# Kernel optimization log

Measured on AMD Instinct MI355X. Metric: run time of the kernel, lower is better.

The kernel has to match this reference:

```python
import jax, jax.numpy as jnp
import numpy as np

B, N, L, S, H, E = 4, 8, 512, 512, 8, 64  # e == d (value head dim)


def setup_inputs() -> dict:
    key = jax.random.key(0)
    ks = jax.random.split(key, 6)
    shp_q = (B, N, L, H, E)
    shp_kv = (B, N, S, H, E)
    return {
        "q_re": jax.random.normal(ks[0], shp_q, dtype=jnp.float32),
        "q_im": jax.random.normal(ks[1], shp_q, dtype=jnp.float32),
        "k_re": jax.random.normal(ks[2], shp_kv, dtype=jnp.float32),
        "k_im": jax.random.normal(ks[3], shp_kv, dtype=jnp.float32),
        "v_re": jax.random.normal(ks[4], shp_kv, dtype=jnp.float32),
        "v_im": jax.random.normal(ks[5], shp_kv, dtype=jnp.float32),
    }


def reference(q_re, q_im, k_re, k_im, v_re, v_im):
    # complex_mul('bnlhe,bnshe->bnhls', q, k):
    #   real = qr.kr - qi.ki ; imag = qr.ki - qi.kr  (note: NOT standard +; faithful to source)
    s_re = (jnp.einsum('bnlhe,bnshe->bnhls', q_re, k_re)
            - jnp.einsum('bnlhe,bnshe->bnhls', q_im, k_im))
    s_im = (jnp.einsum('bnlhe,bnshe->bnhls', q_re, k_im)
            - jnp.einsum('bnlhe,bnshe->bnhls', q_im, k_re))
    # softmax over |scores| along key axis s (no 1/sqrt(e) scaling in source)
    mag = jnp.sqrt(s_re * s_re + s_im * s_im)
    attn = jax.nn.softmax(mag, axis=-1)  # [b,n,h,l,s]; dropout = identity (eval)
    # scores are real-valued after softmax; complex_mul with zero imag reduces to:
    v_out_re = jnp.einsum('bnhls,bnshd->bnlhd', attn, v_re)
    v_out_im = jnp.einsum('bnhls,bnshd->bnlhd', attn, v_im)
    # stack real/imag (torch returns complex tensor) -> [2,b,n,l,h,d]
    return jnp.stack((v_out_re, v_out_im), axis=0)
```

## Files before the change

### kernel.cpp

```cpp
#include <hip/hip_runtime.h>
#include <hip/hip_fp16.h>

typedef _Float16 half8 __attribute__((ext_vector_type(8)));
typedef _Float16 half4 __attribute__((ext_vector_type(4)));
typedef __fp16  fp16x2 __attribute__((ext_vector_type(2)));
typedef float f32x4 __attribute__((ext_vector_type(4)));

#define BB 4
#define NB 8
#define LL 512
#define SS 512
#define HH 8
#define EE 64
#define ROWSTRIDE (HH * EE)

__device__ __forceinline__ unsigned pkh(float a, float b) {
    union { fp16x2 h; unsigned u; } c;
    c.h = __builtin_amdgcn_cvt_pkrtz(a, b);
    return c.u;
}


__global__ __launch_bounds__(512, 4) void cattn_kernel(
    const float* __restrict__ qre, const float* __restrict__ qim,
    const float* __restrict__ kre, const float* __restrict__ kim,
    const float* __restrict__ vre, const float* __restrict__ vim,
    float* __restrict__ out)
{
    __shared__ __align__(16) _Float16 KtRe[2][64 * 64];
    __shared__ __align__(16) _Float16 KtIm[2][64 * 64];
    __shared__ __align__(16) _Float16 VtRe[2][64 * 64];
    __shared__ __align__(16) _Float16 VtIm[2][64 * 64];
    __shared__ __align__(16) _Float16 Pbuf[8][16 * 64];

    const int tid  = threadIdx.x;
    const int wave = tid >> 6;
    const int lane = tid & 63;
    const int lgrp = lane >> 4;
    const int l16  = lane & 15;

    const int bid  = blockIdx.x;
    const int nid  = (bid & 7) * 128 + (bid >> 3);
    const int lt   = nid & 3;
    const int head = nid >> 2;
    const int h    = head & 7;
    const int bn   = head >> 3;

    const size_t headQ = (size_t)bn * LL * ROWSTRIDE + (size_t)h * EE;
    const size_t headK = (size_t)bn * SS * ROWSTRIDE + (size_t)h * EE;

    float4 ka[2], kb[2];
    float4 vv[4];

    const int kEc0  = tid & 7;
    const int kS0   = (tid >> 3) & 63;
    const int vArr  = tid >> 8;
    const int vD0   = (tid & 15) * 4;
    const int vS0   = ((tid >> 4) & 15) * 4;

    auto stage_load = [&](int st) {
        const int tb = st * 64;
        {
            const float* p = kre + headK + (size_t)(tb + kS0) * ROWSTRIDE + kEc0 * 8;
            ka[0] = *(const float4*)p;
            kb[0] = *(const float4*)(p + 4);
        }
        {
            const float* p = kim + headK + (size_t)(tb + kS0) * ROWSTRIDE + kEc0 * 8;
            ka[1] = *(const float4*)p;
            kb[1] = *(const float4*)(p + 4);
        }
        {
            const float* src = vArr ? vim : vre;
            #pragma unroll
            for (int i = 0; i < 4; ++i)
                vv[i] = *(const float4*)(src + headK + (size_t)(tb + vS0 + i) * ROWSTRIDE + vD0);
        }
    };

    auto stage_write = [&](int buf) {
        #pragma unroll
        for (int it = 0; it < 2; ++it) {
            union { half8 h; unsigned u[4]; } kv;
            kv.u[0] = pkh(ka[it].x, ka[it].y);
            kv.u[1] = pkh(ka[it].z, ka[it].w);
            kv.u[2] = pkh(kb[it].x, kb[it].y);
            kv.u[3] = pkh(kb[it].z, kb[it].w);
            _Float16* base = it ? KtIm[buf] : KtRe[buf];
            *reinterpret_cast<half8*>(reinterpret_cast<char*>(base) +
                kS0 * 128 + ((kEc0 * 16) ^ ((kS0 & 7) << 4))) = kv.h;
        }
        {
            _Float16* base = vArr ? VtIm[buf] : VtRe[buf];
            #pragma unroll
            for (int dd = 0; dd < 4; ++dd) {
                int d = vD0 + dd;
                union { half4 h; unsigned u[2]; } hv;
                hv.u[0] = pkh((&vv[0].x)[dd], (&vv[1].x)[dd]);
                hv.u[1] = pkh((&vv[2].x)[dd], (&vv[3].x)[dd]);
                *reinterpret_cast<half4*>(reinterpret_cast<char*>(base) +
                    d * 128 + ((vS0 * 2) ^ ((d & 7) << 4))) = hv.h;
            }
        }
    };

    const int l0 = lt * 128 + wave * 16;
    half8 qr[2], qin[2];
    {
        size_t base = headQ + (size_t)(l0 + l16) * ROWSTRIDE + lgrp * 8;
        #pragma unroll
        for (int ec = 0; ec < 2; ++ec) {
            float4 a0 = *(const float4*)(qre + base + ec * 32);
            float4 a1 = *(const float4*)(qre + base + ec * 32 + 4);
            float4 b0 = *(const float4*)(qim + base + ec * 32);
            float4 b1 = *(const float4*)(qim + base + ec * 32 + 4);
            #pragma unroll
            for (int j = 0; j < 4; ++j) {
                qr[ec][j]      = (_Float16)((&a0.x)[j]);
                qr[ec][4 + j]  = (_Float16)((&a1.x)[j]);
                qin[ec][j]     = (_Float16)(-(&b0.x)[j]);
                qin[ec][4 + j] = (_Float16)(-(&b1.x)[j]);
            }
        }
    }

    f32x4 ore[4], oim[4];
    #pragma unroll
    for (int n = 0; n < 4; ++n) { ore[n] = (f32x4){0.f,0.f,0.f,0.f}; oim[n] = (f32x4){0.f,0.f,0.f,0.f}; }
    float m = -1e30f, lsum = 0.f;

    stage_load(0);
    stage_write(0);
    __syncthreads();

    char* Pw = reinterpret_cast<char*>(&Pbuf[wave][0]);
    const int prow = l16 * 128;
    const int pswz = (l16 & 7) << 4;

    for (int st = 0; st < 8; ++st) {
        const int cur = st & 1;
        if (st < 7) stage_load(st + 1);

        const char* KR = (const char*)KtRe[cur];
        const char* KI = (const char*)KtIm[cur];
        const char* VR = (const char*)VtRe[cur];
        const char* VI = (const char*)VtIm[cur];

        float p_[4][4];
        float tmax = 0.f;
        #pragma unroll
        for (int n = 0; n < 4; ++n) {
            int srow = n * 16 + l16;
            int rb   = srow * 128;
            int swz  = (srow & 7) << 4;
            half8 kr0 = *(const half8*)(KR + rb + ((lgrp * 16)      ^ swz));
            half8 kr1 = *(const half8*)(KR + rb + ((64 + lgrp * 16) ^ swz));
            half8 ki0 = *(const half8*)(KI + rb + ((lgrp * 16)      ^ swz));
            half8 ki1 = *(const half8*)(KI + rb + ((64 + lgrp * 16) ^ swz));
            f32x4 z = (f32x4){0.f,0.f,0.f,0.f};
            z = __builtin_amdgcn_mfma_f32_16x16x32_f16(kr0, qr[0],  z, 0, 0, 0);
            z = __builtin_amdgcn_mfma_f32_16x16x32_f16(kr1, qr[1],  z, 0, 0, 0);
            z = __builtin_amdgcn_mfma_f32_16x16x32_f16(ki0, qin[0], z, 0, 0, 0);
            z = __builtin_amdgcn_mfma_f32_16x16x32_f16(ki1, qin[1], z, 0, 0, 0);
            f32x4 w = (f32x4){0.f,0.f,0.f,0.f};
            w = __builtin_amdgcn_mfma_f32_16x16x32_f16(ki0, qr[0],  w, 0, 0, 0);
            w = __builtin_amdgcn_mfma_f32_16x16x32_f16(ki1, qr[1],  w, 0, 0, 0);
            w = __builtin_amdgcn_mfma_f32_16x16x32_f16(kr0, qin[0], w, 0, 0, 0);
            w = __builtin_amdgcn_mfma_f32_16x16x32_f16(kr1, qin[1], w, 0, 0, 0);
            #pragma unroll
            for (int r = 0; r < 4; ++r) {
                float mg = __builtin_amdgcn_sqrtf(z[r] * z[r] + w[r] * w[r]);
                p_[n][r] = mg;
                tmax = fmaxf(tmax, mg);
            }
        }

        tmax = fmaxf(tmax, __shfl_xor(tmax, 16));
        tmax = fmaxf(tmax, __shfl_xor(tmax, 32));
        float mn = fmaxf(m, tmax);
        if (__any(tmax > m)) {
            float sc = __expf(m - mn);
            lsum *= sc;
            float scr[4];
            #pragma unroll
            for (int r = 0; r < 4; ++r) scr[r] = __shfl(sc, lgrp * 4 + r);
            #pragma unroll
            for (int n = 0; n < 4; ++n)
                #pragma unroll
                for (int r = 0; r < 4; ++r) { ore[n][r] *= scr[r]; oim[n][r] *= scr[r]; }
        }
        m = mn;
        float ps = 0.f;
        #pragma unroll
        for (int n = 0; n < 4; ++n)
            #pragma unroll
            for (int r = 0; r < 4; ++r) {
                float pe = __expf(p_[n][r] - mn);
                p_[n][r] = pe;
                ps += pe;
            }
        ps += __shfl_xor(ps, 16);
        ps += __shfl_xor(ps, 32);
        lsum += ps;

        #pragma unroll
        for (int n = 0; n < 4; ++n) {
            uint2 val;
            val.x = pkh(p_[n][0], p_[n][1]);
            val.y = pkh(p_[n][2], p_[n][3]);
            *reinterpret_cast<uint2*>(Pw + prow + ((n * 32 + lgrp * 8) ^ pswz)) = val;
        }

        #pragma unroll
        for (int kc = 0; kc < 2; ++kc) {
            half8 pa = *reinterpret_cast<const half8*>(Pw + prow + ((kc * 64 + lgrp * 16) ^ pswz));
            int sb2 = (kc * 32 + lgrp * 8) * 2;
            #pragma unroll
            for (int nd = 0; nd < 4; ++nd) {
                int d  = nd * 16 + l16;
                int vo = d * 128 + (sb2 ^ ((d & 7) << 4));
                half8 vr = *(const half8*)(VR + vo);
                half8 vi = *(const half8*)(VI + vo);
                ore[nd] = __builtin_amdgcn_mfma_f32_16x16x32_f16(pa, vr, ore[nd], 0, 0, 0);
                oim[nd] = __builtin_amdgcn_mfma_f32_16x16x32_f16(pa, vi, oim[nd], 0, 0, 0);
            }
        }

        if (st < 7) stage_write(cur ^ 1);
        __syncthreads();
    }

    const size_t outImOff = (size_t)BB * NB * LL * HH * EE;
    #pragma unroll
    for (int r = 0; r < 4; ++r) {
        int lrow = l0 + lgrp * 4 + r;
        float ls  = __shfl(lsum, lgrp * 4 + r);
        float inv = 1.f / ls;
        size_t obase = ((size_t)bn * LL + lrow) * ROWSTRIDE + (size_t)h * EE;
        #pragma unroll
        for (int nd = 0; nd < 4; ++nd) {
            int d = nd * 16 + l16;
            out[obase + d]            = ore[nd][r] * inv;
            out[outImOff + obase + d] = oim[nd][r] * inv;
        }
    }
}

extern "C" void kernel_launch(void* const* d_in, const int* in_sizes, int n_in,
                              void* d_out, int out_size, void* d_ws, size_t ws_size,
                              hipStream_t stream) {
    const float* qre = (const float*)d_in[0];
    const float* qim = (const float*)d_in[1];
    const float* kre = (const float*)d_in[2];
    const float* kim = (const float*)d_in[3];
    const float* vre = (const float*)d_in[4];
    const float* vim = (const float*)d_in[5];
    float* out = (float*)d_out;
    dim3 grid(1024), block(512);
    hipLaunchKernelGGL(cattn_kernel, grid, block, 0, stream,
                       qre, qim, kre, kim, vre, vim, out);
}
```

Measured before the change: 82.36 us.

## Single-buffer K/V shared tiles to cut LDS and raise occupancy

Drops the double-buffered K/V LDS tiles in favor of one buffer each, which roughly halves that part of shared memory. The launch-bounds occupancy hint goes from 4 to 6 blocks per CU. Global loads for the next tile are still issued early and held in registers. The LDS write now sits between two barriers, adding a __syncthreads per iteration, and the higher occupancy target may force register spills.

```diff
diff --git a/kernel.cpp b/kernel.cpp
--- a/kernel.cpp
+++ b/kernel.cpp
@@ -21,16 +21,16 @@
 }
 
 
-__global__ __launch_bounds__(512, 4) void cattn_kernel(
+__global__ __launch_bounds__(512, 6) void cattn_kernel(
     const float* __restrict__ qre, const float* __restrict__ qim,
     const float* __restrict__ kre, const float* __restrict__ kim,
     const float* __restrict__ vre, const float* __restrict__ vim,
     float* __restrict__ out)
 {
-    __shared__ __align__(16) _Float16 KtRe[2][64 * 64];
-    __shared__ __align__(16) _Float16 KtIm[2][64 * 64];
-    __shared__ __align__(16) _Float16 VtRe[2][64 * 64];
-    __shared__ __align__(16) _Float16 VtIm[2][64 * 64];
+    __shared__ __align__(16) _Float16 KtRe[64 * 64];
+    __shared__ __align__(16) _Float16 KtIm[64 * 64];
+    __shared__ __align__(16) _Float16 VtRe[64 * 64];
+    __shared__ __align__(16) _Float16 VtIm[64 * 64];
     __shared__ __align__(16) _Float16 Pbuf[8][16 * 64];
 
     const int tid  = threadIdx.x;
@@ -78,7 +78,7 @@
         }
     };
 
-    auto stage_write = [&](int buf) {
+    auto stage_write = [&]() {
         #pragma unroll
         for (int it = 0; it < 2; ++it) {
             union { half8 h; unsigned u[4]; } kv;
@@ -86,12 +86,12 @@
             kv.u[1] = pkh(ka[it].z, ka[it].w);
             kv.u[2] = pkh(kb[it].x, kb[it].y);
             kv.u[3] = pkh(kb[it].z, kb[it].w);
-            _Float16* base = it ? KtIm[buf] : KtRe[buf];
+            _Float16* base = it ? KtIm : KtRe;
             *reinterpret_cast<half8*>(reinterpret_cast<char*>(base) +
                 kS0 * 128 + ((kEc0 * 16) ^ ((kS0 & 7) << 4))) = kv.h;
         }
         {
-            _Float16* base = vArr ? VtIm[buf] : VtRe[buf];
+            _Float16* base = vArr ? VtIm : VtRe;
             #pragma unroll
             for (int dd = 0; dd < 4; ++dd) {
                 int d = vD0 + dd;
@@ -130,7 +130,7 @@
     float m = -1e30f, lsum = 0.f;
 
     stage_load(0);
-    stage_write(0);
+    stage_write();
     __syncthreads();
 
     char* Pw = reinterpret_cast<char*>(&Pbuf[wave][0]);
@@ -138,13 +138,12 @@
     const int pswz = (l16 & 7) << 4;
 
     for (int st = 0; st < 8; ++st) {
-        const int cur = st & 1;
         if (st < 7) stage_load(st + 1);
 
-        const char* KR = (const char*)KtRe[cur];
-        const char* KI = (const char*)KtIm[cur];
-        const char* VR = (const char*)VtRe[cur];
-        const char* VI = (const char*)VtIm[cur];
+        const char* KR = (const char*)KtRe;
+        const char* KI = (const char*)KtIm;
+        const char* VR = (const char*)VtRe;
+        const char* VI = (const char*)VtIm;
 
         float p_[4][4];
         float tmax = 0.f;
@@ -226,8 +225,11 @@
             }
         }
 
-        if (st < 7) stage_write(cur ^ 1);
         __syncthreads();
+        if (st < 7) {
+            stage_write();
+            __syncthreads();
+        }
     }
 
     const size_t outImOff = (size_t)BB * NB * LL * HH * EE;
```

New measurement: 267.6 us. +224.9%, slower.

## Use 1024-thread blocks covering half a head and move LDS staging earlier

Applied to the files above, without the earlier changes.

Doubles the block size to 16 waves, so each block handles 256 query rows of one head and the grid shrinks to 512 blocks. Each K/V stage is loaded once and shared by twice as many waves, and the per-thread staging load is halved. The write of the next K/V tile into LDS now happens right after the score MFMAs rather than after the PV step, overlapping it with the softmax work. The trade-offs are fewer blocks for the GPU, a larger LDS footprint from 16 P buffers, and launch_bounds(1024,4) that may squeeze registers per thread.

```diff
diff --git a/kernel.cpp b/kernel.cpp
--- a/kernel.cpp
+++ b/kernel.cpp
@@ -21,7 +21,7 @@
 }
 
 
-__global__ __launch_bounds__(512, 4) void cattn_kernel(
+__global__ __launch_bounds__(1024, 4) void cattn_kernel(
     const float* __restrict__ qre, const float* __restrict__ qim,
     const float* __restrict__ kre, const float* __restrict__ kim,
     const float* __restrict__ vre, const float* __restrict__ vim,
@@ -31,7 +31,7 @@
     __shared__ __align__(16) _Float16 KtIm[2][64 * 64];
     __shared__ __align__(16) _Float16 VtRe[2][64 * 64];
     __shared__ __align__(16) _Float16 VtIm[2][64 * 64];
-    __shared__ __align__(16) _Float16 Pbuf[8][16 * 64];
+    __shared__ __align__(16) _Float16 Pbuf[16][16 * 64];
 
     const int tid  = threadIdx.x;
     const int wave = tid >> 6;
@@ -40,60 +40,55 @@
     const int l16  = lane & 15;
 
     const int bid  = blockIdx.x;
-    const int nid  = (bid & 7) * 128 + (bid >> 3);
-    const int lt   = nid & 3;
-    const int head = nid >> 2;
+    const int nid  = (bid & 7) * 64 + (bid >> 3);
+    const int half = nid & 1;
+    const int head = nid >> 1;
     const int h    = head & 7;
     const int bn   = head >> 3;
 
     const size_t headQ = (size_t)bn * LL * ROWSTRIDE + (size_t)h * EE;
     const size_t headK = (size_t)bn * SS * ROWSTRIDE + (size_t)h * EE;
 
-    float4 ka[2], kb[2];
-    float4 vv[4];
-
-    const int kEc0  = tid & 7;
-    const int kS0   = (tid >> 3) & 63;
-    const int vArr  = tid >> 8;
-    const int vD0   = (tid & 15) * 4;
-    const int vS0   = ((tid >> 4) & 15) * 4;
+    float4 ka, kb;
+    float2 vv[4];
+
+    const int kEc0 = tid & 7;
+    const int kS0  = (tid >> 3) & 63;
+    const int kArr = tid >> 9;
+    const int vD0  = (tid & 31) * 2;
+    const int vS0  = ((tid >> 5) & 15) * 4;
+    const int vArr = tid >> 9;
 
     auto stage_load = [&](int st) {
         const int tb = st * 64;
         {
-            const float* p = kre + headK + (size_t)(tb + kS0) * ROWSTRIDE + kEc0 * 8;
-            ka[0] = *(const float4*)p;
-            kb[0] = *(const float4*)(p + 4);
-        }
-        {
-            const float* p = kim + headK + (size_t)(tb + kS0) * ROWSTRIDE + kEc0 * 8;
-            ka[1] = *(const float4*)p;
-            kb[1] = *(const float4*)(p + 4);
+            const float* p = (kArr ? kim : kre) + headK + (size_t)(tb + kS0) * ROWSTRIDE + kEc0 * 8;
+            ka = *(const float4*)p;
+            kb = *(const float4*)(p + 4);
         }
         {
             const float* src = vArr ? vim : vre;
             #pragma unroll
             for (int i = 0; i < 4; ++i)
-                vv[i] = *(const float4*)(src + headK + (size_t)(tb + vS0 + i) * ROWSTRIDE + vD0);
+                vv[i] = *(const float2*)(src + headK + (size_t)(tb + vS0 + i) * ROWSTRIDE + vD0);
         }
     };
 
     auto stage_write = [&](int buf) {
-        #pragma unroll
-        for (int it = 0; it < 2; ++it) {
+        {
             union { half8 h; unsigned u[4]; } kv;
-            kv.u[0] = pkh(ka[it].x, ka[it].y);
-            kv.u[1] = pkh(ka[it].z, ka[it].w);
-            kv.u[2] = pkh(kb[it].x, kb[it].y);
-            kv.u[3] = pkh(kb[it].z, kb[it].w);
-            _Float16* base = it ? KtIm[buf] : KtRe[buf];
+            kv.u[0] = pkh(ka.x, ka.y);
+            kv.u[1] = pkh(ka.z, ka.w);
+            kv.u[2] = pkh(kb.x, kb.y);
+            kv.u[3] = pkh(kb.z, kb.w);
+            _Float16* base = kArr ? KtIm[buf] : KtRe[buf];
             *reinterpret_cast<half8*>(reinterpret_cast<char*>(base) +
                 kS0 * 128 + ((kEc0 * 16) ^ ((kS0 & 7) << 4))) = kv.h;
         }
         {
             _Float16* base = vArr ? VtIm[buf] : VtRe[buf];
             #pragma unroll
-            for (int dd = 0; dd < 4; ++dd) {
+            for (int dd = 0; dd < 2; ++dd) {
                 int d = vD0 + dd;
                 union { half4 h; unsigned u[2]; } hv;
                 hv.u[0] = pkh((&vv[0].x)[dd], (&vv[1].x)[dd]);
@@ -104,7 +99,7 @@
         }
     };
 
-    const int l0 = lt * 128 + wave * 16;
+    const int l0 = half * 256 + wave * 16;
     half8 qr[2], qin[2];
     {
         size_t base = headQ + (size_t)(l0 + l16) * ROWSTRIDE + lgrp * 8;
@@ -175,6 +170,8 @@
             }
         }
 
+        if (st < 7) stage_write(cur ^ 1);
+
         tmax = fmaxf(tmax, __shfl_xor(tmax, 16));
         tmax = fmaxf(tmax, __shfl_xor(tmax, 32));
         float mn = fmaxf(m, tmax);
@@ -226,7 +223,6 @@
             }
         }
 
-        if (st < 7) stage_write(cur ^ 1);
         __syncthreads();
     }
 
@@ -256,7 +252,7 @@
     const float* vre = (const float*)d_in[4];
     const float* vim = (const float*)d_in[5];
     float* out = (float*)d_out;
-    dim3 grid(1024), block(512);
+    dim3 grid(512), block(1024);
     hipLaunchKernelGGL(cattn_kernel, grid, block, 0, stream,
                        qre, qim, kre, kim, vre, vim, out);
 }
```

New measurement: 87.22 us. +5.9%, slower.
